# Performance work log

Measured on AMD Instinct MI355X. Metric: run time of the kernel, lower is better.

Reference implementation:

```python
import jax, jax.numpy as jnp
import numpy as np

B, L, D = 8, 2048, 64

def setup_inputs() -> dict:
    key = jax.random.key(0)
    kq, kk, kv, kqm, kkm = jax.random.split(key, 5)
    return {
        "query": jax.random.normal(kq, (B, L, D), dtype=jnp.float32),
        "key": jax.random.normal(kk, (B, L, D), dtype=jnp.float32),
        "value": jax.random.normal(kv, (B, L, D), dtype=jnp.float32),
        "q_mask": jax.random.randint(kqm, (B, L), 0, 2, dtype=jnp.int32),
        "k_mask": jax.random.randint(kkm, (B, L), 0, 2, dtype=jnp.int32),
    }

def reference(query, key, value, q_mask, k_mask):
    # scale defaults to D_q; divide scores by sqrt(D_q)
    D_q = query.shape[-1]
    qm = q_mask.astype(jnp.float32)  # [B, L_q]
    km = k_mask.astype(jnp.float32)  # [B, L_k]
    # outer-product mask: [B, L_q, L_k]
    mask = qm[:, :, None] * km[:, None, :]
    scores = jnp.einsum("bqd,bkd->bqk", query, key) / jnp.sqrt(jnp.float32(D_q))
    # masked_fill(-inf).exp(): masked positions become exactly 0
    A = jnp.where(mask == 0, 0.0, jnp.exp(scores))  # [B, L_q, L_k]
    # sum clamped to min 1.0 (NOT a standard softmax normalization)
    A_sum = jnp.maximum(A.sum(axis=-1, keepdims=True), 1.0)
    attn = A / A_sum
    return jnp.einsum("bqk,bkd->bqd", attn, value)
```

## Files before the change

kernel.cpp:

```cpp
#include <hip/hip_runtime.h>
#include <hip/hip_bf16.h>
#include <stdint.h>

#define BB 8
#define LL 2048
#define DD 64

typedef short bf16x8 __attribute__((ext_vector_type(8)));
typedef float f32x4 __attribute__((ext_vector_type(4)));
typedef unsigned short ushort_t;
typedef __attribute__((address_space(1))) const unsigned int gas_u32;
typedef __attribute__((address_space(3))) unsigned int las_u32;

__device__ __forceinline__ unsigned pk2(float lo, float hi) {
    union { __hip_bfloat162 h; unsigned u; } c;
    c.h = __float22bfloat162_rn(make_float2(lo, hi));
    return c.u;
}
__device__ __forceinline__ float4 ld4(const float* __restrict__ p) {
    return *reinterpret_cast<const float4*>(p);
}
__device__ __forceinline__ bf16x8 cvt8f(float4 a, float4 b) {
    union { bf16x8 v; unsigned u[4]; } r;
    r.u[0] = pk2(a.x, a.y); r.u[1] = pk2(a.z, a.w);
    r.u[2] = pk2(b.x, b.y); r.u[3] = pk2(b.z, b.w);
    return r.v;
}
__device__ __forceinline__ void glds16(const void* g, void* lds_base_uniform) {
    __builtin_amdgcn_global_load_lds((gas_u32*)g, (las_u32*)lds_base_uniform, 16, 0, 0);
}
__device__ __forceinline__ float bfu2f(unsigned bits) {
    union { unsigned u; float f; } c; c.u = bits << 16; return c.f;
}
__device__ __forceinline__ unsigned f2bf_u(float f) {
    union { float f; unsigned u; } v; v.f = f;
    return (v.u + 0x8000u) >> 16;
}
__device__ __forceinline__ bf16x8 cvt8(const float* __restrict__ p) {
    float4 a = ld4(p), b = ld4(p + 4);
    union { bf16x8 v; unsigned u[4]; } r;
    r.u[0] = f2bf_u(a.x) | (f2bf_u(a.y) << 16);
    r.u[1] = f2bf_u(a.z) | (f2bf_u(a.w) << 16);
    r.u[2] = f2bf_u(b.x) | (f2bf_u(b.y) << 16);
    r.u[3] = f2bf_u(b.z) | (f2bf_u(b.w) << 16);
    return r.v;
}

__global__ __launch_bounds__(256) void pack_k_bf16(const float* __restrict__ K,
                                                   ushort_t* __restrict__ Kb) {
    size_t i = ((size_t)blockIdx.x * 256 + threadIdx.x) * 8;
    float4 a = ld4(K + i), b = ld4(K + i + 4);
    uint4 o = { pk2(a.x, a.y), pk2(a.z, a.w), pk2(b.x, b.y), pk2(b.z, b.w) };
    *reinterpret_cast<uint4*>(Kb + i) = o;
}

__global__ __launch_bounds__(256) void transpose_v_bf(const float* __restrict__ V,
                                                      ushort_t* __restrict__ VT) {
    __shared__ float t[64][65];
    const int b  = blockIdx.x >> 5;
    const int kt = (blockIdx.x & 31) << 6;
    {
        const int r  = threadIdx.x >> 2;
        const int cq = (threadIdx.x & 3) << 4;
        const float* src = V + ((size_t)(b * LL + kt + r)) * DD + cq;
        #pragma unroll
        for (int i = 0; i < 4; ++i) {
            float4 v = ld4(src + 4 * i);
            t[r][cq + 4 * i + 0] = v.x; t[r][cq + 4 * i + 1] = v.y;
            t[r][cq + 4 * i + 2] = v.z; t[r][cq + 4 * i + 3] = v.w;
        }
    }
    __syncthreads();
    {
        const int d  = threadIdx.x >> 2;
        const int kq = (threadIdx.x & 3) << 4;
        ushort_t* dst = VT + ((size_t)(b * DD + d)) * LL + kt + kq;
        #pragma unroll
        for (int u = 0; u < 2; ++u) {
            uint4 o;
            o.x = pk2(t[kq + 8 * u + 0][d], t[kq + 8 * u + 1][d]);
            o.y = pk2(t[kq + 8 * u + 2][d], t[kq + 8 * u + 3][d]);
            o.z = pk2(t[kq + 8 * u + 4][d], t[kq + 8 * u + 5][d]);
            o.w = pk2(t[kq + 8 * u + 6][d], t[kq + 8 * u + 7][d]);
            *reinterpret_cast<uint4*>(dst + 8 * u) = o;
        }
    }
}

__global__ __launch_bounds__(512, 4) void attn8(
    const float* __restrict__ Q,
    const ushort_t* __restrict__ Kbf,
    const ushort_t* __restrict__ VTb,
    const int* __restrict__ kmask,
    float* __restrict__ Opart)
{
    const int tid  = threadIdx.x;
    const int wave = tid >> 6;
    const int lane = tid & 63;
    const int ln   = lane & 15;
    const int quad = lane >> 4;

    const int bx    = blockIdx.x;
    const int ksp   = bx & 3;
    const int qt    = (bx >> 2) & 15;
    const int b     = bx >> 6;
    const int q0    = qt * 128;
    const int kbase = ksp * 512;

    __shared__ char     lds[2][16384];
    __shared__ ushort_t kmbf[512];

    const char* Kg = (const char*)Kbf + (size_t)b * LL * DD * 2;
    const char* Vg = (const char*)VTb + (size_t)b * DD * LL * 2;
    const int gr = tid >> 3;
    const int gc = (tid & 7) ^ (gr & 7);

    #define STAGE(buf, k0)                                                     \
        do {                                                                   \
            glds16(Kg + (size_t)(kbase + (k0) + gr) * 128 + gc * 16,           \
                   &lds[buf][wave * 1024]);                                    \
            glds16(Vg + (size_t)gr * (LL * 2) + (kbase + (k0)) * 2 + gc * 16,  \
                   &lds[buf][8192 + wave * 1024]);                             \
        } while (0)

    STAGE(0, 0);

    if (tid < 128) {
        int4 a = *reinterpret_cast<const int4*>(kmask + b * LL + kbase + tid * 4);
        uint2 u;
        u.x = (a.x ? 0x3F80u : 0u) | ((a.y ? 0x3F80u : 0u) << 16);
        u.y = (a.z ? 0x3F80u : 0u) | ((a.w ? 0x3F80u : 0u) << 16);
        *reinterpret_cast<uint2*>(kmbf + tid * 4) = u;
    }
    bf16x8 qf[2];
    {
        const float* qp = Q + ((size_t)(b * LL + q0 + 16 * wave + ln)) * DD + quad * 8;
        qf[0] = cvt8f(ld4(qp),      ld4(qp + 4));
        qf[1] = cvt8f(ld4(qp + 32), ld4(qp + 36));
    }

    f32x4 Oacc[4] = {{0,0,0,0},{0,0,0,0},{0,0,0,0},{0,0,0,0}};
    float dsum = 0.f;

    const int src0 = ln + ((quad & 1) << 5);
    const int src1 = src0 + 16;
    const bool hi  = quad >= 2;
    const float EC = 0.125f * 1.44269504f;

    for (int it = 0; it < 8; ++it) {
        __syncthreads();
        if (it != 7) STAGE((it + 1) & 1, (it + 1) * 64);

        const char* LK = lds[it & 1];
        const char* LV = lds[it & 1] + 8192;

        bf16x8 kf[4][2];
        #pragma unroll
        for (int tt = 0; tt < 4; ++tt) {
            const int r = 16 * tt + ln;
            #pragma unroll
            for (int dh = 0; dh < 2; ++dh) {
                const int c = (dh * 4 + quad) ^ (ln & 7);
                kf[tt][dh] = *reinterpret_cast<const bf16x8*>(LK + r * 128 + c * 16);
            }
        }
        bf16x8 vf[2][4];
        #pragma unroll
        for (int kh = 0; kh < 2; ++kh) {
            const int c = (kh * 4 + quad) ^ (ln & 7);
            #pragma unroll
            for (int db = 0; db < 4; ++db) {
                const int d = db * 16 + ln;
                vf[kh][db] = *reinterpret_cast<const bf16x8*>(LV + d * 128 + c * 16);
            }
        }

        unsigned w[4][2];
        #pragma unroll
        for (int tt = 0; tt < 4; ++tt) {
            f32x4 acc = (f32x4){0.f, 0.f, 0.f, 0.f};
            acc = __builtin_amdgcn_mfma_f32_16x16x32_bf16(kf[tt][0], qf[0], acc, 0, 0, 0);
            acc = __builtin_amdgcn_mfma_f32_16x16x32_bf16(kf[tt][1], qf[1], acc, 0, 0, 0);
            ushort4 mu = *reinterpret_cast<const ushort4*>(
                kmbf + it * 64 + 16 * tt + 4 * quad);
            float e0 = exp2f(acc[0] * EC) * bfu2f(mu.x);
            float e1 = exp2f(acc[1] * EC) * bfu2f(mu.y);
            float e2 = exp2f(acc[2] * EC) * bfu2f(mu.z);
            float e3 = exp2f(acc[3] * EC) * bfu2f(mu.w);
            dsum += (e0 + e1) + (e2 + e3);
            w[tt][0] = pk2(e0, e1);
            w[tt][1] = pk2(e2, e3);
        }
        #pragma unroll
        for (int g = 0; g < 2; ++g) {
            union { bf16x8 v; unsigned u[4]; } pf;
            unsigned a0 = __shfl(w[2*g][0], src0), b0 = __shfl(w[2*g+1][0], src0);
            unsigned a1 = __shfl(w[2*g][1], src0), b1 = __shfl(w[2*g+1][1], src0);
            unsigned a2 = __shfl(w[2*g][0], src1), b2 = __shfl(w[2*g+1][0], src1);
            unsigned a3 = __shfl(w[2*g][1], src1), b3 = __shfl(w[2*g+1][1], src1);
            pf.u[0] = hi ? b0 : a0;
            pf.u[1] = hi ? b1 : a1;
            pf.u[2] = hi ? b2 : a2;
            pf.u[3] = hi ? b3 : a3;
            #pragma unroll
            for (int db = 0; db < 4; ++db)
                Oacc[db] = __builtin_amdgcn_mfma_f32_16x16x32_bf16(pf.v, vf[g][db], Oacc[db], 0, 0, 0);
        }
    }
    #undef STAGE

    {
        float v = dsum;
        v += __shfl_xor(v, 16);
        v += __shfl_xor(v, 32);
        dsum = v;
    }

    float* pb = Opart + (size_t)bx * 8320;
    #pragma unroll
    for (int db = 0; db < 4; ++db)
        #pragma unroll
        for (int r = 0; r < 4; ++r)
            pb[(16 * wave + quad * 4 + r) * 64 + db * 16 + ln] = Oacc[db][r];
    if (quad == 0) pb[8192 + 16 * wave + ln] = dsum;
}

__global__ __launch_bounds__(256) void reduce_norm(
    const float* __restrict__ Opart,
    const int* __restrict__ qmask,
    float* __restrict__ Out)
{
    const int rb = blockIdx.x;
    const int qt = rb & 15;
    const int b  = rb >> 4;
    const int t  = threadIdx.x;
    const int q  = t >> 1;
    const int d0 = (t & 1) * 32;

    const float* p0 = Opart + (size_t)((b * 16 + qt) * 4 + 0) * 8320;
    const float* p1 = p0 + 8320;
    const float* p2 = p1 + 8320;
    const float* p3 = p2 + 8320;

    float dn = p0[8192 + q] + p1[8192 + q] + p2[8192 + q] + p3[8192 + q];
    float sc = qmask[b * LL + qt * 128 + q] ? (1.0f / fmaxf(dn, 1.0f)) : 0.0f;

    const int off = q * 64 + d0;
    float* op = Out + ((size_t)(b * LL + qt * 128 + q)) * DD + d0;
    #pragma unroll
    for (int i = 0; i < 8; ++i) {
        f32x4 v = *reinterpret_cast<const f32x4*>(p0 + off + 4 * i)
                + *reinterpret_cast<const f32x4*>(p1 + off + 4 * i)
                + *reinterpret_cast<const f32x4*>(p2 + off + 4 * i)
                + *reinterpret_cast<const f32x4*>(p3 + off + 4 * i);
        *reinterpret_cast<f32x4*>(op + 4 * i) = v * sc;
    }
}

__global__ __launch_bounds__(256, 4) void attn_mfma(
    const float* __restrict__ Q, const float* __restrict__ K,
    const float* __restrict__ V, const int* __restrict__ qmask,
    const int* __restrict__ kmask, float* __restrict__ Out)
{
    const int tid  = threadIdx.x;
    const int wave = tid >> 6;
    const int lane = tid & 63;
    const int n    = lane & 15;
    const int quad = lane >> 4;
    const int bx = blockIdx.x;
    const int b  = bx >> 7;
    const int q0 = (bx & 127) << 4;
    __shared__ float Pl[4][576];
    __shared__ float Opart2[4][16][68];
    __shared__ float Denp[4][16];
    const float* Qp = Q + ((size_t)(b * LL + q0 + n)) * DD + quad * 8;
    bf16x8 qf0 = cvt8(Qp);
    bf16x8 qf1 = cvt8(Qp + 32);
    const float* Kb = K + ((size_t)(b * LL) + n) * DD + quad * 8;
    const float* Vb = V + ((size_t)(b * LL) + quad * 8) * DD + n;
    const int* kmb = kmask + b * LL;
    f32x4 Oacc[4] = {{0,0,0,0},{0,0,0,0},{0,0,0,0},{0,0,0,0}};
    float den[4]  = {0.f, 0.f, 0.f, 0.f};
    float*       pw = &Pl[wave][144 * (n >> 3) + 36 * quad + (n & 7)];
    const float* pr = &Pl[wave][9 * lane];
    const int kbeg = wave * (LL / 4);
    const int kend = kbeg + (LL / 4);
    for (int k0 = kbeg; k0 < kend; k0 += 32) {
        const float* krow = Kb + (size_t)k0 * DD;
        bf16x8 kA0 = cvt8(krow);
        bf16x8 kA1 = cvt8(krow + 32);
        bf16x8 kB0 = cvt8(krow + 16 * DD);
        bf16x8 kB1 = cvt8(krow + 16 * DD + 32);
        f32x4 z = {0.f, 0.f, 0.f, 0.f};
        f32x4 S0 = __builtin_amdgcn_mfma_f32_16x16x32_bf16(qf0, kA0, z, 0, 0, 0);
        S0 = __builtin_amdgcn_mfma_f32_16x16x32_bf16(qf1, kA1, S0, 0, 0, 0);
        f32x4 S1 = __builtin_amdgcn_mfma_f32_16x16x32_bf16(qf0, kB0, z, 0, 0, 0);
        S1 = __builtin_amdgcn_mfma_f32_16x16x32_bf16(qf1, kB1, S1, 0, 0, 0);
        float km0 = (float)kmb[k0 + n];
        float km1 = (float)kmb[k0 + 16 + n];
        #pragma unroll
        for (int r = 0; r < 4; ++r) {
            float e0 = __expf(S0[r] * 0.125f) * km0;
            float e1 = __expf(S1[r] * 0.125f) * km1;
            den[r] += e0 + e1;
            pw[9 * r]       = e0;
            pw[288 + 9 * r] = e1;
        }
        __builtin_amdgcn_wave_barrier();
        float pv[8];
        #pragma unroll
        for (int j = 0; j < 8; ++j) pv[j] = pr[j];
        __builtin_amdgcn_wave_barrier();
        union { bf16x8 v; unsigned u[4]; } pf;
        #pragma unroll
        for (int j = 0; j < 4; ++j)
            pf.u[j] = f2bf_u(pv[2 * j]) | (f2bf_u(pv[2 * j + 1]) << 16);
        const float* vrow = Vb + (size_t)k0 * DD;
        #pragma unroll
        for (int db = 0; db < 4; ++db) {
            union { bf16x8 v; unsigned u[4]; } vfr;
            #pragma unroll
            for (int jj = 0; jj < 4; ++jj) {
                unsigned lo  = f2bf_u(vrow[(2 * jj) * DD + db * 16]);
                unsigned hi2 = f2bf_u(vrow[(2 * jj + 1) * DD + db * 16]);
                vfr.u[jj] = lo | (hi2 << 16);
            }
            Oacc[db] = __builtin_amdgcn_mfma_f32_16x16x32_bf16(pf.v, vfr.v, Oacc[db], 0, 0, 0);
        }
    }
    #pragma unroll
    for (int r = 0; r < 4; ++r) {
        float v = den[r];
        v += __shfl_xor(v, 1); v += __shfl_xor(v, 2);
        v += __shfl_xor(v, 4); v += __shfl_xor(v, 8);
        den[r] = v;
    }
    #pragma unroll
    for (int db = 0; db < 4; ++db)
        #pragma unroll
        for (int r = 0; r < 4; ++r)
            Opart2[wave][quad * 4 + r][db * 16 + n] = Oacc[db][r];
    if (n == 0) {
        #pragma unroll
        for (int r = 0; r < 4; ++r) Denp[wave][quad * 4 + r] = den[r];
    }
    __syncthreads();
    const int q  = tid >> 4;
    const int d0 = (tid & 15) * 4;
    f32x4 sum = *reinterpret_cast<const f32x4*>(&Opart2[0][q][d0]);
    sum += *reinterpret_cast<const f32x4*>(&Opart2[1][q][d0]);
    sum += *reinterpret_cast<const f32x4*>(&Opart2[2][q][d0]);
    sum += *reinterpret_cast<const f32x4*>(&Opart2[3][q][d0]);
    float dn  = Denp[0][q] + Denp[1][q] + Denp[2][q] + Denp[3][q];
    float inv = 1.0f / fmaxf(dn, 1.0f);
    float s   = qmask[b * LL + q0 + q] ? inv : 0.0f;
    f32x4 o   = sum * s;
    float* op = Out + ((size_t)(b * LL + q0 + q)) * DD + d0;
    *reinterpret_cast<f32x4*>(op) = o;
}

extern "C" void kernel_launch(void* const* d_in, const int* in_sizes, int n_in,
                              void* d_out, int out_size, void* d_ws, size_t ws_size,
                              hipStream_t stream) {
    (void)in_sizes; (void)n_in; (void)out_size;
    const float* Q  = (const float*)d_in[0];
    const float* K  = (const float*)d_in[1];
    const float* V  = (const float*)d_in[2];
    const int* qm   = (const int*)d_in[3];
    const int* km   = (const int*)d_in[4];
    float* Out      = (float*)d_out;

    const size_t elems   = (size_t)BB * LL * DD;
    const size_t part_off = 4u * 1024 * 1024;
    const size_t ws_need  = part_off + (size_t)512 * 8320 * sizeof(float);
    if (ws_size >= ws_need && d_ws != nullptr) {
        ushort_t* Kbf = (ushort_t*)d_ws;
        ushort_t* VTb = Kbf + elems;
        float* Opart  = (float*)((char*)d_ws + part_off);
        pack_k_bf16   <<<dim3(elems / (256 * 8)), dim3(256), 0, stream>>>(K, Kbf);
        transpose_v_bf<<<dim3(BB * (LL / 64)),    dim3(256), 0, stream>>>(V, VTb);
        attn8<<<dim3(512), dim3(512), 0, stream>>>(Q, Kbf, VTb, km, Opart);
        reduce_norm<<<dim3(128), dim3(256), 0, stream>>>(Opart, qm, Out);
    } else {
        attn_mfma<<<dim3(BB * (LL / 16)), dim3(256), 0, stream>>>(Q, K, V, qm, km, Out);
    }
}
```

Baseline: 106.2 us.

## Fuse K/V prep kernels and split keys across wave pairs with LDS reduction

Merges the K bf16 pack and the V transpose into one prep kernel, saving a launch. The attention kernel now has each pair of waves share two 16-row query slices and split each 128-key tile between them, so every K/V fragment loaded from LDS feeds two query slices. The double-buffered 64-key stage is replaced by a single-buffered 128-key stage, with an extra barrier before the next prefetch. Partial outputs are combined through LDS atomic adds before the global write, which adds LDS use and atomics and removes the overlap of loads with compute.

Result: slower. 150.8 us (+42.0%).

```diff
diff --git a/kernel.cpp b/kernel.cpp
--- a/kernel.cpp
+++ b/kernel.cpp
@@ -46,19 +46,25 @@
     return r.v;
 }
 
-__global__ __launch_bounds__(256) void pack_k_bf16(const float* __restrict__ K,
-                                                   ushort_t* __restrict__ Kb) {
-    size_t i = ((size_t)blockIdx.x * 256 + threadIdx.x) * 8;
-    float4 a = ld4(K + i), b = ld4(K + i + 4);
-    uint4 o = { pk2(a.x, a.y), pk2(a.z, a.w), pk2(b.x, b.y), pk2(b.z, b.w) };
-    *reinterpret_cast<uint4*>(Kb + i) = o;
-}
-
-__global__ __launch_bounds__(256) void transpose_v_bf(const float* __restrict__ V,
-                                                      ushort_t* __restrict__ VT) {
+__global__ __launch_bounds__(256) void prep_kv(const float* __restrict__ K,
+                                               const float* __restrict__ V,
+                                               ushort_t* __restrict__ Kb,
+                                               ushort_t* __restrict__ VT) {
     __shared__ float t[64][65];
     const int b  = blockIdx.x >> 5;
     const int kt = (blockIdx.x & 31) << 6;
+    {
+        const int kr = threadIdx.x >> 2;
+        const int cq = (threadIdx.x & 3) << 4;
+        const float* src = K + ((size_t)(b * LL + kt + kr)) * DD + cq;
+        ushort_t*    dst = Kb + ((size_t)(b * LL + kt + kr)) * DD + cq;
+        #pragma unroll
+        for (int i = 0; i < 2; ++i) {
+            float4 a = ld4(src + 8 * i), c = ld4(src + 8 * i + 4);
+            uint4 o = { pk2(a.x, a.y), pk2(a.z, a.w), pk2(c.x, c.y), pk2(c.z, c.w) };
+            *reinterpret_cast<uint4*>(dst + 8 * i) = o;
+        }
+    }
     {
         const int r  = threadIdx.x >> 2;
         const int cq = (threadIdx.x & 3) << 4;
@@ -87,7 +93,7 @@
     }
 }
 
-__global__ __launch_bounds__(512, 4) void attn8(
+__global__ __launch_bounds__(512, 4) void attn9(
     const float* __restrict__ Q,
     const ushort_t* __restrict__ Kbf,
     const ushort_t* __restrict__ VTb,
@@ -99,6 +105,8 @@
     const int lane = tid & 63;
     const int ln   = lane & 15;
     const int quad = lane >> 4;
+    const int sh   = wave >> 1;
+    const int h    = wave & 1;
 
     const int bx    = blockIdx.x;
     const int ksp   = bx & 3;
@@ -107,122 +115,164 @@
     const int q0    = qt * 128;
     const int kbase = ksp * 512;
 
-    __shared__ char     lds[2][16384];
+    __shared__ char     lds[32768];
+    __shared__ float    Osum[128][68];
+    __shared__ float    Dsum[128];
     __shared__ ushort_t kmbf[512];
 
     const char* Kg = (const char*)Kbf + (size_t)b * LL * DD * 2;
     const char* Vg = (const char*)VTb + (size_t)b * DD * LL * 2;
-    const int gr = tid >> 3;
-    const int gc = (tid & 7) ^ (gr & 7);
-
-    #define STAGE(buf, k0)                                                     \
-        do {                                                                   \
-            glds16(Kg + (size_t)(kbase + (k0) + gr) * 128 + gc * 16,           \
-                   &lds[buf][wave * 1024]);                                    \
-            glds16(Vg + (size_t)gr * (LL * 2) + (kbase + (k0)) * 2 + gc * 16,  \
-                   &lds[buf][8192 + wave * 1024]);                             \
+
+    const int krow0 = wave * 8 + (lane >> 3);
+    const int kscol = (lane & 7) ^ (lane >> 3);
+    const int vrow0 = wave * 4 + (lane >> 4);
+    const int vscol = (lane & 15) ^ (vrow0 & 15);
+
+    #define STAGE(k0)                                                           \
+        do {                                                                    \
+            glds16(Kg + (size_t)(kbase + (k0) + krow0) * 128 + kscol * 16,      \
+                   &lds[wave * 1024]);                                          \
+            glds16(Kg + (size_t)(kbase + (k0) + krow0 + 64) * 128 + kscol * 16, \
+                   &lds[8192 + wave * 1024]);                                   \
+            glds16(Vg + (size_t)vrow0 * (LL * 2) + (kbase + (k0)) * 2 + vscol * 16, \
+                   &lds[16384 + wave * 1024]);                                  \
+            glds16(Vg + (size_t)(vrow0 + 32) * (LL * 2) + (kbase + (k0)) * 2 + vscol * 16, \
+                   &lds[24576 + wave * 1024]);                                  \
         } while (0)
 
-    STAGE(0, 0);
-
+    STAGE(0);
+
+    for (int i = tid; i < 128 * 68; i += 512) (&Osum[0][0])[i] = 0.f;
     if (tid < 128) {
+        Dsum[tid] = 0.f;
         int4 a = *reinterpret_cast<const int4*>(kmask + b * LL + kbase + tid * 4);
         uint2 u;
         u.x = (a.x ? 0x3F80u : 0u) | ((a.y ? 0x3F80u : 0u) << 16);
         u.y = (a.z ? 0x3F80u : 0u) | ((a.w ? 0x3F80u : 0u) << 16);
         *reinterpret_cast<uint2*>(kmbf + tid * 4) = u;
     }
-    bf16x8 qf[2];
-    {
-        const float* qp = Q + ((size_t)(b * LL + q0 + 16 * wave + ln)) * DD + quad * 8;
-        qf[0] = cvt8f(ld4(qp),      ld4(qp + 4));
-        qf[1] = cvt8f(ld4(qp + 32), ld4(qp + 36));
-    }
-
-    f32x4 Oacc[4] = {{0,0,0,0},{0,0,0,0},{0,0,0,0},{0,0,0,0}};
-    float dsum = 0.f;
+    bf16x8 qf[2][2];
+    #pragma unroll
+    for (int sl = 0; sl < 2; ++sl) {
+        const float* qp = Q + ((size_t)(b * LL + q0 + 16 * (2 * sh + sl) + ln)) * DD + quad * 8;
+        qf[sl][0] = cvt8f(ld4(qp),      ld4(qp + 4));
+        qf[sl][1] = cvt8f(ld4(qp + 32), ld4(qp + 36));
+    }
+
+    f32x4 Oacc[2][4];
+    #pragma unroll
+    for (int sl = 0; sl < 2; ++sl)
+        #pragma unroll
+        for (int d = 0; d < 4; ++d) Oacc[sl][d] = (f32x4){0.f, 0.f, 0.f, 0.f};
+    float dsum[2] = {0.f, 0.f};
 
     const int src0 = ln + ((quad & 1) << 5);
     const int src1 = src0 + 16;
     const bool hi  = quad >= 2;
     const float EC = 0.125f * 1.44269504f;
 
-    for (int it = 0; it < 8; ++it) {
+    for (int it = 0; it < 4; ++it) {
         __syncthreads();
-        if (it != 7) STAGE((it + 1) & 1, (it + 1) * 64);
-
-        const char* LK = lds[it & 1];
-        const char* LV = lds[it & 1] + 8192;
+
+        const char* LK = lds;
+        const char* LV = lds + 16384;
 
         bf16x8 kf[4][2];
         #pragma unroll
         for (int tt = 0; tt < 4; ++tt) {
-            const int r = 16 * tt + ln;
+            const int r = 64 * h + 16 * tt + ln;
             #pragma unroll
             for (int dh = 0; dh < 2; ++dh) {
                 const int c = (dh * 4 + quad) ^ (ln & 7);
                 kf[tt][dh] = *reinterpret_cast<const bf16x8*>(LK + r * 128 + c * 16);
             }
         }
+
+        unsigned w2[2][4][2];
+        #pragma unroll
+        for (int sl = 0; sl < 2; ++sl) {
+            #pragma unroll
+            for (int tt = 0; tt < 4; ++tt) {
+                f32x4 acc = (f32x4){0.f, 0.f, 0.f, 0.f};
+                acc = __builtin_amdgcn_mfma_f32_16x16x32_bf16(kf[tt][0], qf[sl][0], acc, 0, 0, 0);
+                acc = __builtin_amdgcn_mfma_f32_16x16x32_bf16(kf[tt][1], qf[sl][1], acc, 0, 0, 0);
+                ushort4 mu = *reinterpret_cast<const ushort4*>(
+                    kmbf + it * 128 + 64 * h + 16 * tt + 4 * quad);
+                float e0 = exp2f(acc[0] * EC) * bfu2f(mu.x);
+                float e1 = exp2f(acc[1] * EC) * bfu2f(mu.y);
+                float e2 = exp2f(acc[2] * EC) * bfu2f(mu.z);
+                float e3 = exp2f(acc[3] * EC) * bfu2f(mu.w);
+                dsum[sl] += (e0 + e1) + (e2 + e3);
+                w2[sl][tt][0] = pk2(e0, e1);
+                w2[sl][tt][1] = pk2(e2, e3);
+            }
+        }
+
         bf16x8 vf[2][4];
         #pragma unroll
-        for (int kh = 0; kh < 2; ++kh) {
-            const int c = (kh * 4 + quad) ^ (ln & 7);
+        for (int g = 0; g < 2; ++g) {
+            const int c = (8 * h + 4 * g + quad) ^ ln;
             #pragma unroll
             for (int db = 0; db < 4; ++db) {
                 const int d = db * 16 + ln;
-                vf[kh][db] = *reinterpret_cast<const bf16x8*>(LV + d * 128 + c * 16);
+                vf[g][db] = *reinterpret_cast<const bf16x8*>(LV + d * 256 + c * 16);
             }
         }
 
-        unsigned w[4][2];
-        #pragma unroll
-        for (int tt = 0; tt < 4; ++tt) {
-            f32x4 acc = (f32x4){0.f, 0.f, 0.f, 0.f};
-            acc = __builtin_amdgcn_mfma_f32_16x16x32_bf16(kf[tt][0], qf[0], acc, 0, 0, 0);
-            acc = __builtin_amdgcn_mfma_f32_16x16x32_bf16(kf[tt][1], qf[1], acc, 0, 0, 0);
-            ushort4 mu = *reinterpret_cast<const ushort4*>(
-                kmbf + it * 64 + 16 * tt + 4 * quad);
-            float e0 = exp2f(acc[0] * EC) * bfu2f(mu.x);
-            float e1 = exp2f(acc[1] * EC) * bfu2f(mu.y);
-            float e2 = exp2f(acc[2] * EC) * bfu2f(mu.z);
-            float e3 = exp2f(acc[3] * EC) * bfu2f(mu.w);
-            dsum += (e0 + e1) + (e2 + e3);
-            w[tt][0] = pk2(e0, e1);
-            w[tt][1] = pk2(e2, e3);
-        }
-        #pragma unroll
-        for (int g = 0; g < 2; ++g) {
-            union { bf16x8 v; unsigned u[4]; } pf;
-            unsigned a0 = __shfl(w[2*g][0], src0), b0 = __shfl(w[2*g+1][0], src0);
-            unsigned a1 = __shfl(w[2*g][1], src0), b1 = __shfl(w[2*g+1][1], src0);
-            unsigned a2 = __shfl(w[2*g][0], src1), b2 = __shfl(w[2*g+1][0], src1);
-            unsigned a3 = __shfl(w[2*g][1], src1), b3 = __shfl(w[2*g+1][1], src1);
-            pf.u[0] = hi ? b0 : a0;
-            pf.u[1] = hi ? b1 : a1;
-            pf.u[2] = hi ? b2 : a2;
-            pf.u[3] = hi ? b3 : a3;
-            #pragma unroll
-            for (int db = 0; db < 4; ++db)
-                Oacc[db] = __builtin_amdgcn_mfma_f32_16x16x32_bf16(pf.v, vf[g][db], Oacc[db], 0, 0, 0);
-        }
+        #pragma unroll
+        for (int sl = 0; sl < 2; ++sl) {
+            #pragma unroll
+            for (int g = 0; g < 2; ++g) {
+                union { bf16x8 v; unsigned u[4]; } pf;
+                unsigned a0 = __shfl(w2[sl][2*g][0], src0), b0 = __shfl(w2[sl][2*g+1][0], src0);
+                unsigned a1 = __shfl(w2[sl][2*g][1], src0), b1 = __shfl(w2[sl][2*g+1][1], src0);
+                unsigned a2 = __shfl(w2[sl][2*g][0], src1), b2 = __shfl(w2[sl][2*g+1][0], src1);
+                unsigned a3 = __shfl(w2[sl][2*g][1], src1), b3 = __shfl(w2[sl][2*g+1][1], src1);
+                pf.u[0] = hi ? b0 : a0;
+                pf.u[1] = hi ? b1 : a1;
+                pf.u[2] = hi ? b2 : a2;
+                pf.u[3] = hi ? b3 : a3;
+                #pragma unroll
+                for (int db = 0; db < 4; ++db)
+                    Oacc[sl][db] = __builtin_amdgcn_mfma_f32_16x16x32_bf16(pf.v, vf[g][db], Oacc[sl][db], 0, 0, 0);
+            }
+        }
+
+        __syncthreads();
+        if (it != 3) STAGE((it + 1) * 128);
     }
     #undef STAGE
 
-    {
-        float v = dsum;
+    #pragma unroll
+    for (int sl = 0; sl < 2; ++sl) {
+        float v = dsum[sl];
         v += __shfl_xor(v, 16);
         v += __shfl_xor(v, 32);
-        dsum = v;
-    }
+        dsum[sl] = v;
+    }
+
+    #pragma unroll
+    for (int sl = 0; sl < 2; ++sl) {
+        const int qs = 2 * sh + sl;
+        #pragma unroll
+        for (int db = 0; db < 4; ++db)
+            #pragma unroll
+            for (int r = 0; r < 4; ++r)
+                atomicAdd(&Osum[16 * qs + quad * 4 + r][db * 16 + ln], Oacc[sl][db][r]);
+        if (quad == 0) atomicAdd(&Dsum[16 * qs + ln], dsum[sl]);
+    }
+    __syncthreads();
 
     float* pb = Opart + (size_t)bx * 8320;
-    #pragma unroll
-    for (int db = 0; db < 4; ++db)
-        #pragma unroll
-        for (int r = 0; r < 4; ++r)
-            pb[(16 * wave + quad * 4 + r) * 64 + db * 16 + ln] = Oacc[db][r];
-    if (quad == 0) pb[8192 + 16 * wave + ln] = dsum;
+    {
+        const int q  = tid >> 2;
+        const int d0 = (tid & 3) << 4;
+        #pragma unroll
+        for (int i = 0; i < 4; ++i)
+            *reinterpret_cast<f32x4*>(pb + q * 64 + d0 + 4 * i) =
+                *reinterpret_cast<const f32x4*>(&Osum[q][d0 + 4 * i]);
+    }
+    if (tid < 128) pb[8192 + tid] = Dsum[tid];
 }
 
 __global__ __launch_bounds__(256) void reduce_norm(
@@ -370,16 +420,15 @@
     const int* km   = (const int*)d_in[4];
     float* Out      = (float*)d_out;
 
-    const size_t elems   = (size_t)BB * LL * DD;
+    const size_t elems    = (size_t)BB * LL * DD;
     const size_t part_off = 4u * 1024 * 1024;
     const size_t ws_need  = part_off + (size_t)512 * 8320 * sizeof(float);
     if (ws_size >= ws_need && d_ws != nullptr) {
         ushort_t* Kbf = (ushort_t*)d_ws;
         ushort_t* VTb = Kbf + elems;
         float* Opart  = (float*)((char*)d_ws + part_off);
-        pack_k_bf16   <<<dim3(elems / (256 * 8)), dim3(256), 0, stream>>>(K, Kbf);
-        transpose_v_bf<<<dim3(BB * (LL / 64)),    dim3(256), 0, stream>>>(V, VTb);
-        attn8<<<dim3(512), dim3(512), 0, stream>>>(Q, Kbf, VTb, km, Opart);
+        prep_kv<<<dim3(BB * (LL / 64)), dim3(256), 0, stream>>>(K, V, Kbf, VTb);
+        attn9<<<dim3(512), dim3(512), 0, stream>>>(Q, Kbf, VTb, km, Opart);
         reduce_norm<<<dim3(128), dim3(256), 0, stream>>>(Opart, qm, Out);
     } else {
         attn_mfma<<<dim3(BB * (LL / 16)), dim3(256), 0, stream>>>(Q, K, V, qm, km, Out);
```
